# Kernel tuning notes

Hardware: AMD Instinct MI355X
Metric: run time of the kernel (lower is better)

Reference implementation:

```python
import jax, jax.numpy as jnp
import numpy as np
from jax import lax

DM, DS, K, EXPAND = 512, 16, 4, 1
DI = EXPAND * DM           # d_inner
DT_RANK = (DM + 15) // 16  # ceil(d_model/16) = 32
B, L = 4, 2048


def setup_inputs() -> dict:
    key = jax.random.key(0)
    ks = jax.random.split(key, 10)
    x = jax.random.normal(ks[0], (B, L, DM), dtype=jnp.float32)
    W_in = jax.random.normal(ks[1], (2 * DI, DM), dtype=jnp.float32) * (1.0 / np.sqrt(DM))
    conv_w = jax.random.normal(ks[2], (DI, 1, K), dtype=jnp.float32) * (1.0 / np.sqrt(K))
    conv_b = jax.random.normal(ks[3], (DI,), dtype=jnp.float32) * 0.02
    W_xproj = jax.random.normal(ks[4], (DT_RANK + 2 * DS, DI), dtype=jnp.float32) * (1.0 / np.sqrt(DI))
    W_dt = jax.random.normal(ks[5], (DI, DT_RANK), dtype=jnp.float32) * (1.0 / np.sqrt(DT_RANK))
    b_dt = jax.random.uniform(ks[6], (DI,), dtype=jnp.float32, minval=-4.0, maxval=-2.0)  # softplus(b)~small dt
    A_log = jnp.log(jnp.broadcast_to(jnp.arange(1, DS + 1, dtype=jnp.float32), (DI, DS)))
    D_param = jnp.ones((DI,), dtype=jnp.float32)
    W_out = jax.random.normal(ks[7], (DM, DI), dtype=jnp.float32) * (1.0 / np.sqrt(DI))
    return {"x": x, "W_in": W_in, "conv_w": conv_w, "conv_b": conv_b,
            "W_xproj": W_xproj, "W_dt": W_dt, "b_dt": b_dt,
            "A_log": A_log, "D_param": D_param, "W_out": W_out}


def _mamba(x, W_in, conv_w, conv_b, W_xproj, W_dt, b_dt, A_log, D_param, W_out):
    # in_proj -> x, z branches [B,L,DI] each
    xz = jnp.einsum('bld,ed->ble', x, W_in)
    xc, z = xz[..., :DI], xz[..., DI:]
    # causal depthwise conv1d over time
    xt = jnp.transpose(xc, (0, 2, 1))                      # [B,DI,L]
    xt = jnp.pad(xt, ((0, 0), (0, 0), (K - 1, 0)))
    xt = lax.conv_general_dilated(xt, conv_w, (1,), 'VALID',
                                  dimension_numbers=('NCH', 'OIH', 'NCH'),
                                  feature_group_count=DI)
    xt = xt + conv_b[None, :, None]
    xc = jax.nn.silu(jnp.transpose(xt, (0, 2, 1)))         # [B,L,DI]
    # input-dependent dt, B, C
    x_dbl = jnp.einsum('bld,ed->ble', xc, W_xproj)         # [B,L,DT_RANK+2*DS]
    dt = x_dbl[..., :DT_RANK]
    Bm = x_dbl[..., DT_RANK:DT_RANK + DS]                  # [B,L,DS]
    Cm = x_dbl[..., DT_RANK + DS:]                         # [B,L,DS]
    dt = jax.nn.softplus(jnp.einsum('blr,dr->bld', dt, W_dt) + b_dt)  # [B,L,DI]
    A = -jnp.exp(A_log)                                    # [DI,DS]
    deltaA = jnp.exp(dt[..., None] * A)                    # [B,L,DI,DS]
    deltaBu = dt[..., None] * Bm[:, :, None, :] * xc[..., None]       # [B,L,DI,DS]

    def step(h, inp):
        dA_t, dBu_t, C_t = inp                             # [B,DI,DS],[B,DI,DS],[B,DS]
        h = dA_t * h + dBu_t
        y = jnp.einsum('bds,bs->bd', h, C_t)
        return h, y

    h0 = jnp.zeros((x.shape[0], DI, DS), dtype=x.dtype)
    _, ys = lax.scan(step, h0, (jnp.transpose(deltaA, (1, 0, 2, 3)),
                                jnp.transpose(deltaBu, (1, 0, 2, 3)),
                                jnp.transpose(Cm, (1, 0, 2))))
    y = jnp.transpose(ys, (1, 0, 2)) + xc * D_param        # [B,L,DI]
    y = y * jax.nn.silu(z)
    out = jnp.einsum('bld,ed->ble', y, W_out)              # [B,L,DM]
    out = jnp.clip(out, -1000.0, 1000.0)
    out = jnp.nan_to_num(out, nan=0.0, posinf=1000.0, neginf=-1000.0)
    return out


def reference(x, W_in, conv_w, conv_b, W_xproj, W_dt, b_dt, A_log, D_param, W_out):
    return _mamba(x, W_in, conv_w, conv_b, W_xproj, W_dt, b_dt, A_log, D_param, W_out)
```

## Files before the change

### kernel.cpp

```cpp
#include <hip/hip_runtime.h>
#include <math.h>

#define DMc   512
#define DIc   512
#define DSc   16
#define KCc   4
#define DTRc  32
#define NXDc  64
#define LLEN  2048
#define BBc   4
#define BLT   (BBc*LLEN)

#define NCH   64
#define CLEN  (LLEN/NCH)

typedef __attribute__((ext_vector_type(8))) short short8;
typedef __attribute__((ext_vector_type(8))) unsigned short ushort8;
typedef __attribute__((ext_vector_type(4))) float f32x4;

__device__ __forceinline__ float sigmoidf_(float x) { return 1.f / (1.f + __expf(-x)); }

__device__ __forceinline__ unsigned short f2bf(float x) {
    unsigned int u = __float_as_uint(x);
    u = (u + 0x7FFFu + ((u >> 16) & 1u)) >> 16;
    return (unsigned short)u;
}

__global__ __launch_bounds__(256) void f32_to_bf16_kernel(const float* __restrict__ in,
                                                          unsigned short* __restrict__ out,
                                                          int n8)
{
    int i = blockIdx.x * 256 + threadIdx.x;
    if (i >= n8) return;
    float4 a = ((const float4*)in)[2 * i];
    float4 b = ((const float4*)in)[2 * i + 1];
    ushort8 o;
    o[0] = f2bf(a.x); o[1] = f2bf(a.y); o[2] = f2bf(a.z); o[3] = f2bf(a.w);
    o[4] = f2bf(b.x); o[5] = f2bf(b.y); o[6] = f2bf(b.z); o[7] = f2bf(b.w);
    ((ushort8*)out)[i] = o;
}

template<int EPI>
__global__ __launch_bounds__(256) void gemm_bt_f32(const float* __restrict__ A,
                                                   const float* __restrict__ Bw,
                                                   const float* __restrict__ bias,
                                                   float* __restrict__ C,
                                                   int M, int N, int Kd,
                                                   int lda, int ldb)
{
    __shared__ float As[16][68];
    __shared__ float Bs[16][68];
    const int tid  = threadIdx.x;
    const int tx   = tid & 15;
    const int ty   = tid >> 4;
    const int arow = tid >> 2;
    const int akq  = (tid & 3) << 2;

    const float* Ab = A  + (size_t)(blockIdx.y * 64 + arow) * lda + akq;
    const float* Bb = Bw + (size_t)(blockIdx.x * 64 + arow) * ldb + akq;

    float acc[4][4] = {};

    for (int k0 = 0; k0 < Kd; k0 += 16) {
        float4 av = *(const float4*)(Ab + k0);
        float4 bv = *(const float4*)(Bb + k0);
        __syncthreads();
        As[akq + 0][arow] = av.x; As[akq + 1][arow] = av.y;
        As[akq + 2][arow] = av.z; As[akq + 3][arow] = av.w;
        Bs[akq + 0][arow] = bv.x; Bs[akq + 1][arow] = bv.y;
        Bs[akq + 2][arow] = bv.z; Bs[akq + 3][arow] = bv.w;
        __syncthreads();
#pragma unroll
        for (int k = 0; k < 16; ++k) {
            float4 a = *(const float4*)&As[k][ty << 2];
            float4 b = *(const float4*)&Bs[k][tx << 2];
            float ar[4] = {a.x, a.y, a.z, a.w};
            float br[4] = {b.x, b.y, b.z, b.w};
#pragma unroll
            for (int i = 0; i < 4; ++i)
#pragma unroll
                for (int j = 0; j < 4; ++j)
                    acc[i][j] += ar[i] * br[j];
        }
    }

    float4 bv = make_float4(0.f, 0.f, 0.f, 0.f);
    if (EPI == 2) bv = *(const float4*)(bias + blockIdx.x * 64 + (tx << 2));
#pragma unroll
    for (int i = 0; i < 4; ++i) {
        float v[4] = {acc[i][0], acc[i][1], acc[i][2], acc[i][3]};
        if (EPI == 2) {
            float bb[4] = {bv.x, bv.y, bv.z, bv.w};
#pragma unroll
            for (int j = 0; j < 4; ++j) {
                float s = v[j] + bb[j];
                v[j] = fmaxf(s, 0.f) + log1pf(__expf(-fabsf(s)));
            }
        }
        *(float4*)(C + (size_t)(blockIdx.y * 64 + (ty << 2) + i) * N
                     + blockIdx.x * 64 + (tx << 2)) = make_float4(v[0], v[1], v[2], v[3]);
    }
}

template<int EPI>
__global__ __launch_bounds__(256) void gemm_mfma(const unsigned short* __restrict__ A,
                                                 const unsigned short* __restrict__ Bw,
                                                 float* __restrict__ C,
                                                 int M, int N, int Kd)
{
    __shared__ short As[128][40];
    __shared__ short Bs[128][40];
    const int tid  = threadIdx.x;
    const int lane = tid & 63;
    const int wv   = tid >> 6;
    const int wr   = wv >> 1;
    const int wc   = wv & 1;
    const int fr   = lane & 15;
    const int fq   = lane >> 4;

    const int rowA0 = blockIdx.y * 128;
    const int rowB0 = blockIdx.x * 128;

    const int r0 = tid >> 2,        s0 = (tid & 3) << 3;
    const int r1 = (tid + 256) >> 2, s1 = s0;

    f32x4 acc[4][4];
#pragma unroll
    for (int m = 0; m < 4; ++m)
#pragma unroll
        for (int n = 0; n < 4; ++n) acc[m][n] = (f32x4){0.f, 0.f, 0.f, 0.f};

    for (int k0 = 0; k0 < Kd; k0 += 32) {
        short8 a0 = *(const short8*)(A  + (size_t)(rowA0 + r0) * Kd + k0 + s0);
        short8 a1 = *(const short8*)(A  + (size_t)(rowA0 + r1) * Kd + k0 + s1);
        short8 b0 = *(const short8*)(Bw + (size_t)(rowB0 + r0) * Kd + k0 + s0);
        short8 b1 = *(const short8*)(Bw + (size_t)(rowB0 + r1) * Kd + k0 + s1);
        __syncthreads();
        *(short8*)&As[r0][s0] = a0;
        *(short8*)&As[r1][s1] = a1;
        *(short8*)&Bs[r0][s0] = b0;
        *(short8*)&Bs[r1][s1] = b1;
        __syncthreads();

        short8 af[4], bf[4];
#pragma unroll
        for (int m = 0; m < 4; ++m)
            af[m] = *(const short8*)&As[wr * 64 + m * 16 + fr][fq << 3];
#pragma unroll
        for (int n = 0; n < 4; ++n)
            bf[n] = *(const short8*)&Bs[wc * 64 + n * 16 + fr][fq << 3];
#pragma unroll
        for (int m = 0; m < 4; ++m)
#pragma unroll
            for (int n = 0; n < 4; ++n)
                acc[m][n] = __builtin_amdgcn_mfma_f32_16x16x32_bf16(af[m], bf[n], acc[m][n], 0, 0, 0);
    }

    const int crow0 = rowA0 + wr * 64 + (fq << 2);
    const int ccol0 = rowB0 + wc * 64 + fr;
#pragma unroll
    for (int m = 0; m < 4; ++m)
#pragma unroll
        for (int n = 0; n < 4; ++n)
#pragma unroll
            for (int j = 0; j < 4; ++j) {
                float v = acc[m][n][j];
                if (EPI) v = (v != v) ? 0.f : fminf(fmaxf(v, -1000.f), 1000.f);
                C[(size_t)(crow0 + m * 16 + j) * N + ccol0 + n * 16] = v;
            }
}

__global__ __launch_bounds__(256) void conv_silu_kernel(const float* __restrict__ xz,
                                                        const float* __restrict__ cw,
                                                        const float* __restrict__ cb,
                                                        float* __restrict__ xc)
{
    int gid = blockIdx.x * 256 + threadIdx.x;
    int d = gid & (DIc - 1);
    int l = (gid >> 9) & (LLEN - 1);
    int b = gid >> 20;
    float s = cb[d];
#pragma unroll
    for (int k = 0; k < KCc; ++k) {
        int ls = l + k - (KCc - 1);
        if (ls >= 0)
            s += xz[((size_t)(b * LLEN + ls) << 10) + d] * cw[d * KCc + k];
    }
    xc[gid] = s * sigmoidf_(s);
}

__device__ __forceinline__ size_t hend_off(int b, int c, int s, int d) {
    return ((size_t)((b * NCH + c) * DSc + s) << 10) + d;
}
__device__ __forceinline__ size_t sdt_off(int b, int c, int d) {
    return ((size_t)(4096 + b * NCH + c) << 10) + d;
}

__global__ __launch_bounds__(256) void scan_phase1(const float* __restrict__ dty,
                                                   const float* __restrict__ xc,
                                                   const float* __restrict__ xdbl,
                                                   float* __restrict__ xzbuf,
                                                   const float* __restrict__ A_log)
{
    int half = blockIdx.x & 1;
    int c    = (blockIdx.x >> 1) & (NCH - 1);
    int b    = blockIdx.x >> 7;
    int d    = (half << 8) + threadIdx.x;

    float A[DSc];
#pragma unroll
    for (int s = 0; s < DSc; ++s) A[s] = -__expf(A_log[d * DSc + s]);

    float h[DSc];
#pragma unroll
    for (int s = 0; s < DSc; ++s) h[s] = 0.f;
    float Sdt = 0.f;

    int row0 = b * LLEN + c * CLEN;
    for (int t = 0; t < CLEN; ++t) {
        int row = row0 + t;
        float dtv = dty[((size_t)row << 9) + d];
        float xcv = xc[((size_t)row << 9) + d];
        Sdt += dtv;
        float dBx = dtv * xcv;
        const float* xd = xdbl + (size_t)row * NXDc;
#pragma unroll
        for (int s = 0; s < DSc; ++s)
            h[s] = __expf(dtv * A[s]) * h[s] + dBx * xd[DTRc + s];
    }
#pragma unroll
    for (int s = 0; s < DSc; ++s) xzbuf[hend_off(b, c, s, d)] = h[s];
    xzbuf[sdt_off(b, c, d)] = Sdt;
}

__global__ __launch_bounds__(256) void scan_phase2(float* __restrict__ xzbuf,
                                                   const float* __restrict__ A_log)
{
    int b = blockIdx.x >> 1;
    int d = ((blockIdx.x & 1) << 8) + threadIdx.x;

    float A[DSc];
#pragma unroll
    for (int s = 0; s < DSc; ++s) A[s] = -__expf(A_log[d * DSc + s]);

    float h[DSc];
#pragma unroll
    for (int s = 0; s < DSc; ++s) h[s] = 0.f;

    for (int c = 0; c < NCH; ++c) {
        float Sdt = xzbuf[sdt_off(b, c, d)];
#pragma unroll
        for (int s = 0; s < DSc; ++s) {
            size_t o = hend_off(b, c, s, d);
            float he = xzbuf[o];
            xzbuf[o] = h[s];
            h[s] = __expf(A[s] * Sdt) * h[s] + he;
        }
    }
}

__global__ __launch_bounds__(256) void scan_phase3(const float* __restrict__ dty,
                                                   const float* __restrict__ xc,
                                                   const float* __restrict__ xdbl,
                                                   const float* __restrict__ xzbuf,
                                                   const float* __restrict__ A_log,
                                                   const float* __restrict__ Dp,
                                                   unsigned short* __restrict__ yb)
{
    int half = blockIdx.x & 1;
    int c    = (blockIdx.x >> 1) & (NCH - 1);
    int b    = blockIdx.x >> 7;
    int d    = (half << 8) + threadIdx.x;

    float A[DSc];
#pragma unroll
    for (int s = 0; s < DSc; ++s) A[s] = -__expf(A_log[d * DSc + s]);
    float Dv = Dp[d];

    float h[DSc];
#pragma unroll
    for (int s = 0; s < DSc; ++s) h[s] = xzbuf[hend_off(b, c, s, d)];

    int row0 = b * LLEN + c * CLEN;
    for (int t = 0; t < CLEN; ++t) {
        int row = row0 + t;
        float dtv = dty[((size_t)row << 9) + d];
        float xcv = xc[((size_t)row << 9) + d];
        float zv  = xzbuf[((size_t)row << 10) + DIc + d];
        float dBx = dtv * xcv;
        const float* xd = xdbl + (size_t)row * NXDc;
        float acc = 0.f;
#pragma unroll
        for (int s = 0; s < DSc; ++s) {
            float dA = __expf(dtv * A[s]);
            h[s] = dA * h[s] + dBx * xd[DTRc + s];
            acc += h[s] * xd[DTRc + DSc + s];
        }
        float yv = (acc + xcv * Dv) * (zv * sigmoidf_(zv));
        yb[((size_t)row << 9) + d] = f2bf(yv);
    }
}

extern "C" void kernel_launch(void* const* d_in, const int* in_sizes, int n_in,
                              void* d_out, int out_size, void* d_ws, size_t ws_size,
                              hipStream_t stream)
{
    const float* x      = (const float*)d_in[0];
    const float* W_in   = (const float*)d_in[1];
    const float* conv_w = (const float*)d_in[2];
    const float* conv_b = (const float*)d_in[3];
    const float* W_xp   = (const float*)d_in[4];
    const float* W_dt   = (const float*)d_in[5];
    const float* b_dt   = (const float*)d_in[6];
    const float* A_log  = (const float*)d_in[7];
    const float* D_par  = (const float*)d_in[8];
    const float* W_out  = (const float*)d_in[9];
    float* out = (float*)d_out;

    float* ws   = (float*)d_ws;
    float* xz   = ws;
    float* xc   = xz + (size_t)BLT * 1024;
    float* xdbl = xc + (size_t)BLT * DIc;
    float* dty  = xdbl + (size_t)BLT * NXDc;
    unsigned short* xb  = (unsigned short*)(dty + (size_t)BLT * DIc);
    unsigned short* Wb  = xb + (size_t)BLT * DIc;
    unsigned short* Wob = Wb + (size_t)1024 * DMc;

    f32_to_bf16_kernel<<<(BLT * DMc / 8) / 256, 256, 0, stream>>>(x, xb, BLT * DMc / 8);
    f32_to_bf16_kernel<<<(1024 * DMc / 8) / 256, 256, 0, stream>>>(W_in, Wb, 1024 * DMc / 8);
    f32_to_bf16_kernel<<<(DMc * DIc / 8) / 256, 256, 0, stream>>>(W_out, Wob, DMc * DIc / 8);

    gemm_mfma<0><<<dim3(1024 / 128, BLT / 128), 256, 0, stream>>>(xb, Wb, xz, BLT, 1024, DMc);

    conv_silu_kernel<<<(BLT * DIc) / 256, 256, 0, stream>>>(xz, conv_w, conv_b, xc);

    gemm_bt_f32<0><<<dim3(1, BLT / 64), 256, 0, stream>>>(xc, W_xp, nullptr, xdbl,
                                                          BLT, NXDc, DIc, DIc, DIc);

    gemm_bt_f32<2><<<dim3(DIc / 64, BLT / 64), 256, 0, stream>>>(xdbl, W_dt, b_dt, dty,
                                                                 BLT, DIc, DTRc, NXDc, DTRc);

    scan_phase1<<<BBc * NCH * 2, 256, 0, stream>>>(dty, xc, xdbl, xz, A_log);
    scan_phase2<<<BBc * 2, 256, 0, stream>>>(xz, A_log);
    scan_phase3<<<BBc * NCH * 2, 256, 0, stream>>>(dty, xc, xdbl, xz, A_log, D_par, xb);

    gemm_mfma<1><<<dim3(DMc / 128, BLT / 128), 256, 0, stream>>>(xb, Wob, out, BLT, DMc, DMc);
}
```

Before: 196.0 us.

## Fuse dt projection into scan phases, double chunk count, parallelize phase2 per state

Removes the separate dt GEMM and its BLT×DI buffer. Phase 1 and phase 3 now recompute the dt dot product and softplus per row from xdbl and W_dt held in registers. The number of scan chunks doubles to raise parallelism, and phase 2 now uses one thread per (b,s,d) instead of looping over s. The three bf16 conversion launches are merged into one kernel. This trades extra per-thread FLOPs and register pressure for less memory traffic and fewer launches.

```diff
diff --git a/kernel.cpp b/kernel.cpp
--- a/kernel.cpp
+++ b/kernel.cpp
@@ -11,7 +11,7 @@
 #define BBc   4
 #define BLT   (BBc*LLEN)
 
-#define NCH   64
+#define NCH   128
 #define CLEN  (LLEN/NCH)
 
 typedef __attribute__((ext_vector_type(8))) short short8;
@@ -26,24 +26,32 @@
     return (unsigned short)u;
 }
 
-__global__ __launch_bounds__(256) void f32_to_bf16_kernel(const float* __restrict__ in,
-                                                          unsigned short* __restrict__ out,
-                                                          int n8)
+#define CN1 (BLT * DMc / 8)
+#define CN2 (1024 * DMc / 8)
+#define CN3 (DMc * DIc / 8)
+__global__ __launch_bounds__(256) void convert3_kernel(const float* __restrict__ x,
+                                                       const float* __restrict__ Win,
+                                                       const float* __restrict__ Wout,
+                                                       unsigned short* __restrict__ xb,
+                                                       unsigned short* __restrict__ Wb,
+                                                       unsigned short* __restrict__ Wob)
 {
     int i = blockIdx.x * 256 + threadIdx.x;
-    if (i >= n8) return;
-    float4 a = ((const float4*)in)[2 * i];
-    float4 b = ((const float4*)in)[2 * i + 1];
+    const float* src; unsigned short* dst;
+    if (i < CN1)                  { src = x;    dst = xb;  }
+    else if (i < CN1 + CN2)       { src = Win;  dst = Wb;  i -= CN1; }
+    else if (i < CN1 + CN2 + CN3) { src = Wout; dst = Wob; i -= CN1 + CN2; }
+    else return;
+    float4 a = ((const float4*)src)[2 * i];
+    float4 b = ((const float4*)src)[2 * i + 1];
     ushort8 o;
     o[0] = f2bf(a.x); o[1] = f2bf(a.y); o[2] = f2bf(a.z); o[3] = f2bf(a.w);
     o[4] = f2bf(b.x); o[5] = f2bf(b.y); o[6] = f2bf(b.z); o[7] = f2bf(b.w);
-    ((ushort8*)out)[i] = o;
-}
-
-template<int EPI>
+    ((ushort8*)dst)[i] = o;
+}
+
 __global__ __launch_bounds__(256) void gemm_bt_f32(const float* __restrict__ A,
                                                    const float* __restrict__ Bw,
-                                                   const float* __restrict__ bias,
                                                    float* __restrict__ C,
                                                    int M, int N, int Kd,
                                                    int lda, int ldb)
@@ -84,21 +92,11 @@
         }
     }
 
-    float4 bv = make_float4(0.f, 0.f, 0.f, 0.f);
-    if (EPI == 2) bv = *(const float4*)(bias + blockIdx.x * 64 + (tx << 2));
 #pragma unroll
     for (int i = 0; i < 4; ++i) {
-        float v[4] = {acc[i][0], acc[i][1], acc[i][2], acc[i][3]};
-        if (EPI == 2) {
-            float bb[4] = {bv.x, bv.y, bv.z, bv.w};
-#pragma unroll
-            for (int j = 0; j < 4; ++j) {
-                float s = v[j] + bb[j];
-                v[j] = fmaxf(s, 0.f) + log1pf(__expf(-fabsf(s)));
-            }
-        }
+        float4 v = make_float4(acc[i][0], acc[i][1], acc[i][2], acc[i][3]);
         *(float4*)(C + (size_t)(blockIdx.y * 64 + (ty << 2) + i) * N
-                     + blockIdx.x * 64 + (tx << 2)) = make_float4(v[0], v[1], v[2], v[3]);
+                     + blockIdx.x * 64 + (tx << 2)) = v;
     }
 }
 
@@ -189,27 +187,30 @@
     xc[gid] = s * sigmoidf_(s);
 }
 
-__device__ __forceinline__ size_t hend_off(int b, int c, int s, int d) {
-    return ((size_t)((b * NCH + c) * DSc + s) << 10) + d;
-}
-__device__ __forceinline__ size_t sdt_off(int b, int c, int d) {
-    return ((size_t)(4096 + b * NCH + c) << 10) + d;
-}
-
-__global__ __launch_bounds__(256) void scan_phase1(const float* __restrict__ dty,
-                                                   const float* __restrict__ xc,
+__device__ __forceinline__ size_t hs_off(int b, int c, int s, int d) {
+    return ((size_t)((b * NCH + c) * DSc + s) << 9) + d;
+}
+
+__global__ __launch_bounds__(256) void scan_phase1(const float* __restrict__ xc,
                                                    const float* __restrict__ xdbl,
-                                                   float* __restrict__ xzbuf,
-                                                   const float* __restrict__ A_log)
+                                                   const float* __restrict__ Wdt,
+                                                   const float* __restrict__ bdt,
+                                                   const float* __restrict__ A_log,
+                                                   float* __restrict__ hstate,
+                                                   float* __restrict__ sdtbuf)
 {
     int half = blockIdx.x & 1;
     int c    = (blockIdx.x >> 1) & (NCH - 1);
-    int b    = blockIdx.x >> 7;
+    int b    = blockIdx.x >> 8;
     int d    = (half << 8) + threadIdx.x;
 
     float A[DSc];
 #pragma unroll
     for (int s = 0; s < DSc; ++s) A[s] = -__expf(A_log[d * DSc + s]);
+    float wdt[DTRc];
+#pragma unroll
+    for (int i = 0; i < DTRc; ++i) wdt[i] = Wdt[d * DTRc + i];
+    float bd = bdt[d];
 
     float h[DSc];
 #pragma unroll
@@ -219,76 +220,82 @@
     int row0 = b * LLEN + c * CLEN;
     for (int t = 0; t < CLEN; ++t) {
         int row = row0 + t;
-        float dtv = dty[((size_t)row << 9) + d];
+        const float* xd = xdbl + (size_t)row * NXDc;
+        float sdot = bd;
+#pragma unroll
+        for (int i = 0; i < DTRc; ++i) sdot += xd[i] * wdt[i];
+        float dtv = fmaxf(sdot, 0.f) + log1pf(__expf(-fabsf(sdot)));
         float xcv = xc[((size_t)row << 9) + d];
         Sdt += dtv;
         float dBx = dtv * xcv;
-        const float* xd = xdbl + (size_t)row * NXDc;
 #pragma unroll
         for (int s = 0; s < DSc; ++s)
             h[s] = __expf(dtv * A[s]) * h[s] + dBx * xd[DTRc + s];
     }
 #pragma unroll
-    for (int s = 0; s < DSc; ++s) xzbuf[hend_off(b, c, s, d)] = h[s];
-    xzbuf[sdt_off(b, c, d)] = Sdt;
-}
-
-__global__ __launch_bounds__(256) void scan_phase2(float* __restrict__ xzbuf,
-                                                   const float* __restrict__ A_log)
-{
-    int b = blockIdx.x >> 1;
-    int d = ((blockIdx.x & 1) << 8) + threadIdx.x;
-
-    float A[DSc];
-#pragma unroll
-    for (int s = 0; s < DSc; ++s) A[s] = -__expf(A_log[d * DSc + s]);
-
-    float h[DSc];
-#pragma unroll
-    for (int s = 0; s < DSc; ++s) h[s] = 0.f;
-
+    for (int s = 0; s < DSc; ++s) hstate[hs_off(b, c, s, d)] = h[s];
+    sdtbuf[((size_t)(b * NCH + c) << 9) + d] = Sdt;
+}
+
+__global__ __launch_bounds__(64) void scan_phase2(float* __restrict__ hstate,
+                                                  const float* __restrict__ sdtbuf,
+                                                  const float* __restrict__ A_log)
+{
+    int gid = blockIdx.x * 64 + threadIdx.x;
+    int d = gid & (DIc - 1);
+    int s = (gid >> 9) & (DSc - 1);
+    int b = gid >> 13;
+
+    float A = -__expf(A_log[d * DSc + s]);
+    float h = 0.f;
     for (int c = 0; c < NCH; ++c) {
-        float Sdt = xzbuf[sdt_off(b, c, d)];
-#pragma unroll
-        for (int s = 0; s < DSc; ++s) {
-            size_t o = hend_off(b, c, s, d);
-            float he = xzbuf[o];
-            xzbuf[o] = h[s];
-            h[s] = __expf(A[s] * Sdt) * h[s] + he;
-        }
-    }
-}
-
-__global__ __launch_bounds__(256) void scan_phase3(const float* __restrict__ dty,
-                                                   const float* __restrict__ xc,
+        size_t o = hs_off(b, c, s, d);
+        float he  = hstate[o];
+        float Sdt = sdtbuf[((size_t)(b * NCH + c) << 9) + d];
+        hstate[o] = h;
+        h = __expf(A * Sdt) * h + he;
+    }
+}
+
+__global__ __launch_bounds__(256) void scan_phase3(const float* __restrict__ xc,
                                                    const float* __restrict__ xdbl,
+                                                   const float* __restrict__ Wdt,
+                                                   const float* __restrict__ bdt,
                                                    const float* __restrict__ xzbuf,
+                                                   const float* __restrict__ hstate,
                                                    const float* __restrict__ A_log,
                                                    const float* __restrict__ Dp,
                                                    unsigned short* __restrict__ yb)
 {
     int half = blockIdx.x & 1;
     int c    = (blockIdx.x >> 1) & (NCH - 1);
-    int b    = blockIdx.x >> 7;
+    int b    = blockIdx.x >> 8;
     int d    = (half << 8) + threadIdx.x;
 
     float A[DSc];
 #pragma unroll
     for (int s = 0; s < DSc; ++s) A[s] = -__expf(A_log[d * DSc + s]);
+    float wdt[DTRc];
+#pragma unroll
+    for (int i = 0; i < DTRc; ++i) wdt[i] = Wdt[d * DTRc + i];
+    float bd = bdt[d];
     float Dv = Dp[d];
 
     float h[DSc];
 #pragma unroll
-    for (int s = 0; s < DSc; ++s) h[s] = xzbuf[hend_off(b, c, s, d)];
+    for (int s = 0; s < DSc; ++s) h[s] = hstate[hs_off(b, c, s, d)];
 
     int row0 = b * LLEN + c * CLEN;
     for (int t = 0; t < CLEN; ++t) {
         int row = row0 + t;
-        float dtv = dty[((size_t)row << 9) + d];
+        const float* xd = xdbl + (size_t)row * NXDc;
+        float sdot = bd;
+#pragma unroll
+        for (int i = 0; i < DTRc; ++i) sdot += xd[i] * wdt[i];
+        float dtv = fmaxf(sdot, 0.f) + log1pf(__expf(-fabsf(sdot)));
         float xcv = xc[((size_t)row << 9) + d];
         float zv  = xzbuf[((size_t)row << 10) + DIc + d];
         float dBx = dtv * xcv;
-        const float* xd = xdbl + (size_t)row * NXDc;
         float acc = 0.f;
 #pragma unroll
         for (int s = 0; s < DSc; ++s) {
@@ -321,28 +328,27 @@
     float* xz   = ws;
     float* xc   = xz + (size_t)BLT * 1024;
     float* xdbl = xc + (size_t)BLT * DIc;
-    float* dty  = xdbl + (size_t)BLT * NXDc;
-    unsigned short* xb  = (unsigned short*)(dty + (size_t)BLT * DIc);
+    unsigned short* xb  = (unsigned short*)(xdbl + (size_t)BLT * NXDc);
     unsigned short* Wb  = xb + (size_t)BLT * DIc;
     unsigned short* Wob = Wb + (size_t)1024 * DMc;
-
-    f32_to_bf16_kernel<<<(BLT * DMc / 8) / 256, 256, 0, stream>>>(x, xb, BLT * DMc / 8);
-    f32_to_bf16_kernel<<<(1024 * DMc / 8) / 256, 256, 0, stream>>>(W_in, Wb, 1024 * DMc / 8);
-    f32_to_bf16_kernel<<<(DMc * DIc / 8) / 256, 256, 0, stream>>>(W_out, Wob, DMc * DIc / 8);
+    float* hstate = (float*)(Wob + (size_t)DMc * DIc);
+    float* sdtbuf = hstate + (size_t)BBc * NCH * DSc * DIc;
+
+    convert3_kernel<<<(CN1 + CN2 + CN3 + 255) / 256, 256, 0, stream>>>(
+        x, W_in, W_out, xb, Wb, Wob);
 
     gemm_mfma<0><<<dim3(1024 / 128, BLT / 128), 256, 0, stream>>>(xb, Wb, xz, BLT, 1024, DMc);
 
     conv_silu_kernel<<<(BLT * DIc) / 256, 256, 0, stream>>>(xz, conv_w, conv_b, xc);
 
-    gemm_bt_f32<0><<<dim3(1, BLT / 64), 256, 0, stream>>>(xc, W_xp, nullptr, xdbl,
-                                                          BLT, NXDc, DIc, DIc, DIc);
-
-    gemm_bt_f32<2><<<dim3(DIc / 64, BLT / 64), 256, 0, stream>>>(xdbl, W_dt, b_dt, dty,
-                                                                 BLT, DIc, DTRc, NXDc, DTRc);
-
-    scan_phase1<<<BBc * NCH * 2, 256, 0, stream>>>(dty, xc, xdbl, xz, A_log);
-    scan_phase2<<<BBc * 2, 256, 0, stream>>>(xz, A_log);
-    scan_phase3<<<BBc * NCH * 2, 256, 0, stream>>>(dty, xc, xdbl, xz, A_log, D_par, xb);
+    gemm_bt_f32<<<dim3(1, BLT / 64), 256, 0, stream>>>(xc, W_xp, xdbl,
+                                                       BLT, NXDc, DIc, DIc, DIc);
+
+    scan_phase1<<<BBc * NCH * 2, 256, 0, stream>>>(xc, xdbl, W_dt, b_dt, A_log,
+                                                   hstate, sdtbuf);
+    scan_phase2<<<(BBc * DSc * DIc) / 64, 64, 0, stream>>>(hstate, sdtbuf, A_log);
+    scan_phase3<<<BBc * NCH * 2, 256, 0, stream>>>(xc, xdbl, W_dt, b_dt, xz,
+                                                   hstate, A_log, D_par, xb);
 
     gemm_mfma<1><<<dim3(DMc / 128, BLT / 128), 256, 0, stream>>>(xb, Wob, out, BLT, DMc, DMc);
 }
```

Measured after the change: 181.6 us. -7.4%, faster.
